# Kernel tuning notes

Measured on AMD Instinct MI355X. Metric: run time of the kernel, lower is better.

Reference implementation:

```python
import jax, jax.numpy as jnp
import numpy as np

N = 8192        # nodes
D_IN = 256      # in_dims
D_OUT = 32      # out_dims (assignment clusters)


def setup_inputs() -> dict:
    key = jax.random.key(0)
    k1, k2, k3 = jax.random.split(key, 3)
    main_feat = jax.random.normal(k1, (N, D_IN), dtype=jnp.float32)
    main_adj = jax.random.uniform(k2, (N, N), dtype=jnp.float32)
    W = jax.random.normal(k3, (D_IN, D_OUT), dtype=jnp.float32) * (1.0 / np.sqrt(D_IN))
    b = jnp.zeros((D_OUT,), dtype=jnp.float32)
    return {"main_feat": main_feat, "main_adj": main_adj, "W": W, "b": b}


def reference(main_feat, main_adj, W, b):
    # GraphConvolution: support = X @ W ; out = A @ support + b   -> [N, D_OUT]
    support = main_feat @ W
    assign = main_adj @ support + b
    # softmax over the NODE axis (dim 0), matching F.softmax(main_assign, 0)
    assign = jax.nn.softmax(assign, axis=0)
    # pooling: raw_emb = assign^T @ X  -> [D_OUT, D_IN]
    raw_emb = assign.T @ main_feat
    return raw_emb
```

## Files before the change

kernel.cpp:

```cpp
#include <hip/hip_runtime.h>
#include <stdint.h>

#define NN   8192
#define DIN  256
#define DOUT 32

typedef short bf16x8 __attribute__((ext_vector_type(8)));
typedef float f32x16 __attribute__((ext_vector_type(16)));

union BF8 { uint32_t u[4]; bf16x8 v; };

__device__ __forceinline__ void split_pair(float a, float b, uint32_t& hp, uint32_t& lp) {
    uint32_t ua = __float_as_uint(a), ub = __float_as_uint(b);
    hp = (ua >> 16) | (ub & 0xffff0000u);
    float la = a - __uint_as_float(ua & 0xffff0000u);
    float lb = b - __uint_as_float(ub & 0xffff0000u);
    lp = (__float_as_uint(la) >> 16) | (__float_as_uint(lb) & 0xffff0000u);
}

__global__ __launch_bounds__(256) void k1_support(
    const float* __restrict__ X, const float* __restrict__ W,
    unsigned short* __restrict__ hi_frag, unsigned short* __restrict__ lo_frag)
{
    __shared__ float Xs[32 * 256];
    int t = threadIdx.x;
    int kbase = blockIdx.x * 32;

    const float4* Xg = (const float4*)(X + (size_t)kbase * DIN);
    float4* Xs4 = (float4*)Xs;
#pragma unroll
    for (int p = 0; p < 8; ++p) Xs4[p * 256 + t] = Xg[p * 256 + t];
    __syncthreads();

    int c = t & 31;
    int q = t >> 5;
    int kb2  = q >> 2;
    int half = (q >> 1) & 1;
    int j4   = q & 1;
    int krow0 = kb2 * 16 + half * 8 + j4 * 4;

    float acc[4] = {0.f, 0.f, 0.f, 0.f};
    for (int d = 0; d < 256; ++d) {
        float w = W[d * 32 + c];
#pragma unroll
        for (int jj = 0; jj < 4; ++jj)
            acc[jj] += Xs[(krow0 + jj) * 256 + d] * w;
    }

    uint32_t h01, l01, h23, l23;
    split_pair(acc[0], acc[1], h01, l01);
    split_pair(acc[2], acc[3], h23, l23);

    int ks = (kbase >> 4) + kb2;
    size_t elembase = (size_t)ks * 512 + (size_t)(half * 32 + c) * 8 + j4 * 4;
    *(uint2*)(hi_frag + elembase) = make_uint2(h01, h23);
    *(uint2*)(lo_frag + elembase) = make_uint2(l01, l23);
}

__global__ __launch_bounds__(256) void k2_logits(
    const float* __restrict__ adj,
    const unsigned short* __restrict__ hi_frag,
    const unsigned short* __restrict__ lo_frag,
    float* __restrict__ part)
{
    int t = threadIdx.x;
    int lane = t & 63, wv = t >> 6;
    int row_tile = blockIdx.x * 128 + wv * 32;
    int r  = lane & 31;
    int hs = lane >> 5;

    const float* arow = adj + (size_t)(row_tile + r) * NN + blockIdx.y * 512 + hs * 8;
    const unsigned short* hp = hi_frag + (size_t)blockIdx.y * 32 * 512 + lane * 8;
    const unsigned short* lp = lo_frag + (size_t)blockIdx.y * 32 * 512 + lane * 8;

    f32x16 acc;
#pragma unroll
    for (int i = 0; i < 16; ++i) acc[i] = 0.f;

#pragma unroll 4
    for (int s = 0; s < 32; ++s) {
        float4 a0 = *(const float4*)arow;
        float4 a1 = *(const float4*)(arow + 4);
        BF8 bh, bl, ah, al;
        bh.v = *(const bf16x8*)hp;
        bl.v = *(const bf16x8*)lp;
        split_pair(a0.x, a0.y, ah.u[0], al.u[0]);
        split_pair(a0.z, a0.w, ah.u[1], al.u[1]);
        split_pair(a1.x, a1.y, ah.u[2], al.u[2]);
        split_pair(a1.z, a1.w, ah.u[3], al.u[3]);
        acc = __builtin_amdgcn_mfma_f32_32x32x16_bf16(ah.v, bh.v, acc, 0, 0, 0);
        acc = __builtin_amdgcn_mfma_f32_32x32x16_bf16(ah.v, bl.v, acc, 0, 0, 0);
        acc = __builtin_amdgcn_mfma_f32_32x32x16_bf16(al.v, bh.v, acc, 0, 0, 0);
        arow += 16; hp += 512; lp += 512;
    }

    float* pdst = part + (size_t)blockIdx.y * (NN * DOUT);
#pragma unroll
    for (int reg = 0; reg < 16; ++reg) {
        int rt = (reg & 3) + 8 * (reg >> 2) + 4 * hs;
        pdst[(size_t)(row_tile + rt) * 32 + r] = acc[reg];
    }
}

__global__ __launch_bounds__(256) void k3a_sum_max(
    const float* __restrict__ part, float* __restrict__ logits_sum,
    float* __restrict__ Mpart)
{
    __shared__ float red[256 * 4];
    int t = threadIdx.x;
    size_t base4 = (size_t)blockIdx.x * 1024;

    float mx[4] = {-3.4e38f, -3.4e38f, -3.4e38f, -3.4e38f};
#pragma unroll
    for (int k = 0; k < 4; ++k) {
        size_t f = base4 + k * 256 + t;
        float4 v = ((const float4*)part)[f];
#pragma unroll
        for (int p = 1; p < 16; ++p) {
            float4 u = ((const float4*)(part + (size_t)p * NN * DOUT))[f];
            v.x += u.x; v.y += u.y; v.z += u.z; v.w += u.w;
        }
        ((float4*)logits_sum)[f] = v;
        mx[0] = fmaxf(mx[0], v.x); mx[1] = fmaxf(mx[1], v.y);
        mx[2] = fmaxf(mx[2], v.z); mx[3] = fmaxf(mx[3], v.w);
    }
#pragma unroll
    for (int j = 0; j < 4; ++j) red[t * 4 + j] = mx[j];
    __syncthreads();
    for (int s = 128; s >= 8; s >>= 1) {
        if (t < s)
#pragma unroll
            for (int j = 0; j < 4; ++j)
                red[t * 4 + j] = fmaxf(red[t * 4 + j], red[(t + s) * 4 + j]);
        __syncthreads();
    }
    if (t < 8)
#pragma unroll
        for (int j = 0; j < 4; ++j)
            Mpart[blockIdx.x * 32 + t * 4 + j] = red[t * 4 + j];
}

__global__ __launch_bounds__(256) void k3b_exp_sum(
    const float* __restrict__ logits_sum, const float* __restrict__ Mpart,
    float* __restrict__ e_buf, float* __restrict__ Spart)
{
    __shared__ float Ms[32];
    __shared__ float red[256 * 4];
    int t = threadIdx.x;

    if (t < 32) {
        float m = -3.4e38f;
        for (int g = 0; g < 64; ++g) m = fmaxf(m, Mpart[g * 32 + t]);
        Ms[t] = m;
    }
    __syncthreads();

    int g = t & 7;
    float m0 = Ms[4 * g], m1 = Ms[4 * g + 1], m2 = Ms[4 * g + 2], m3 = Ms[4 * g + 3];
    size_t base4 = (size_t)blockIdx.x * 1024;
    float sm[4] = {0.f, 0.f, 0.f, 0.f};
#pragma unroll
    for (int k = 0; k < 4; ++k) {
        size_t f = base4 + k * 256 + t;
        float4 v = ((const float4*)logits_sum)[f];
        v.x = __expf(v.x - m0); v.y = __expf(v.y - m1);
        v.z = __expf(v.z - m2); v.w = __expf(v.w - m3);
        ((float4*)e_buf)[f] = v;
        sm[0] += v.x; sm[1] += v.y; sm[2] += v.z; sm[3] += v.w;
    }
#pragma unroll
    for (int j = 0; j < 4; ++j) red[t * 4 + j] = sm[j];
    __syncthreads();
    for (int s = 128; s >= 8; s >>= 1) {
        if (t < s)
#pragma unroll
            for (int j = 0; j < 4; ++j)
                red[t * 4 + j] += red[(t + s) * 4 + j];
        __syncthreads();
    }
    if (t < 8)
#pragma unroll
        for (int j = 0; j < 4; ++j)
            Spart[blockIdx.x * 32 + t * 4 + j] = red[t * 4 + j];
}

__global__ __launch_bounds__(256) void k4_pool(
    const float* __restrict__ X, const float* __restrict__ e_buf,
    const float* __restrict__ Spart, float* __restrict__ p4)
{
    __shared__ float Xs[8 * 256];
    __shared__ float As[8 * 32];
    __shared__ float invS[32];
    int t = threadIdx.x;
    int c = t & 31, dg = t >> 5;
    int ibase = blockIdx.x * 64;

    if (t < 32) {
        float s = 0.f;
        for (int g = 0; g < 64; ++g) s += Spart[g * 32 + t];
        invS[t] = 1.0f / s;
    }

    float acc[32];
#pragma unroll
    for (int i = 0; i < 32; ++i) acc[i] = 0.f;

    for (int rnd = 0; rnd < 8; ++rnd) {
        __syncthreads();
        const float4* Xg = (const float4*)(X + (size_t)(ibase + rnd * 8) * DIN);
        float4* Xs4 = (float4*)Xs;
        Xs4[t]       = Xg[t];
        Xs4[256 + t] = Xg[256 + t];
        As[t] = e_buf[(size_t)(ibase + rnd * 8 + (t >> 5)) * 32 + (t & 31)] * invS[t & 31];
        __syncthreads();
#pragma unroll
        for (int i2 = 0; i2 < 8; ++i2) {
            float a = As[i2 * 32 + c];
#pragma unroll
            for (int dd = 0; dd < 32; ++dd)
                acc[dd] += a * Xs[i2 * 256 + dg * 32 + dd];
        }
    }
    float* dst = p4 + (size_t)blockIdx.x * (DOUT * DIN) + (size_t)c * 256 + dg * 32;
#pragma unroll
    for (int v = 0; v < 8; ++v)
        ((float4*)dst)[v] = make_float4(acc[v * 4], acc[v * 4 + 1], acc[v * 4 + 2], acc[v * 4 + 3]);
}

__global__ __launch_bounds__(256) void k5_reduce(
    const float* __restrict__ p4, float* __restrict__ out)
{
    int j = blockIdx.x * 256 + threadIdx.x;
    float a = 0.f;
    for (int g = 0; g < 128; ++g) a += p4[(size_t)g * (DOUT * DIN) + j];
    out[j] = a;
}

extern "C" void kernel_launch(void* const* d_in, const int* in_sizes, int n_in,
                              void* d_out, int out_size, void* d_ws, size_t ws_size,
                              hipStream_t stream) {
    const float* X   = (const float*)d_in[0];
    const float* adj = (const float*)d_in[1];
    const float* W   = (const float*)d_in[2];
    float* out = (float*)d_out;

    char* w = (char*)d_ws;
    unsigned short* hi_frag = (unsigned short*)w;
    unsigned short* lo_frag = (unsigned short*)(w + 512 * 1024);
    float* part       = (float*)(w + 1 * 1024 * 1024);
    float* logits_sum = (float*)(w + 17 * 1024 * 1024);
    float* e_buf      = (float*)(w + 18 * 1024 * 1024);
    float* Mpart      = (float*)(w + 19 * 1024 * 1024);
    float* Spart      = (float*)(w + 19 * 1024 * 1024 + 8192);
    float* p4         = (float*)(w + 19 * 1024 * 1024 + 16384);

    k1_support<<<NN / 32, 256, 0, stream>>>(X, W, hi_frag, lo_frag);
    k2_logits<<<dim3(NN / 128, 16), 256, 0, stream>>>(adj, hi_frag, lo_frag, part);
    k3a_sum_max<<<64, 256, 0, stream>>>(part, logits_sum, Mpart);
    k3b_exp_sum<<<64, 256, 0, stream>>>(logits_sum, Mpart, e_buf, Spart);
    k4_pool<<<128, 256, 0, stream>>>(X, e_buf, Spart, p4);
    k5_reduce<<<DOUT * DIN / 256, 256, 0, stream>>>(p4, out);
}
```

Before: 439.3 us.

## Halve split-K chunks, widen softmax grids, defer normalization to final reduce

The adjacency GEMM now splits K into 8 chunks of 1024 instead of 16 of 512. This halves the partial-logit buffer written by k2 and read by k3a, at the cost of fewer blocks (512 instead of 1024) in the dominant kernel. The softmax max and exp kernels now run 256 blocks with one float4 per thread, and k3b reduces the 256 partial maxima with a tree. Division by the softmax sum moves from k4_pool into k5_reduce, which reduces Spart per output column and scales the result once.

Result: no change. 443.3 us (+0.9%).

```diff
diff --git a/kernel.cpp b/kernel.cpp
--- a/kernel.cpp
+++ b/kernel.cpp
@@ -4,6 +4,8 @@
 #define NN   8192
 #define DIN  256
 #define DOUT 32
+#define NCHUNK 8
+#define NP4   128
 
 typedef short bf16x8 __attribute__((ext_vector_type(8)));
 typedef float f32x16 __attribute__((ext_vector_type(16)));
@@ -69,16 +71,16 @@
     int r  = lane & 31;
     int hs = lane >> 5;
 
-    const float* arow = adj + (size_t)(row_tile + r) * NN + blockIdx.y * 512 + hs * 8;
-    const unsigned short* hp = hi_frag + (size_t)blockIdx.y * 32 * 512 + lane * 8;
-    const unsigned short* lp = lo_frag + (size_t)blockIdx.y * 32 * 512 + lane * 8;
+    const float* arow = adj + (size_t)(row_tile + r) * NN + blockIdx.y * 1024 + hs * 8;
+    const unsigned short* hp = hi_frag + (size_t)blockIdx.y * 64 * 512 + lane * 8;
+    const unsigned short* lp = lo_frag + (size_t)blockIdx.y * 64 * 512 + lane * 8;
 
     f32x16 acc;
 #pragma unroll
     for (int i = 0; i < 16; ++i) acc[i] = 0.f;
 
 #pragma unroll 4
-    for (int s = 0; s < 32; ++s) {
+    for (int s = 0; s < 64; ++s) {
         float4 a0 = *(const float4*)arow;
         float4 a1 = *(const float4*)(arow + 4);
         BF8 bh, bl, ah, al;
@@ -108,24 +110,18 @@
 {
     __shared__ float red[256 * 4];
     int t = threadIdx.x;
-    size_t base4 = (size_t)blockIdx.x * 1024;
-
-    float mx[4] = {-3.4e38f, -3.4e38f, -3.4e38f, -3.4e38f};
-#pragma unroll
-    for (int k = 0; k < 4; ++k) {
-        size_t f = base4 + k * 256 + t;
-        float4 v = ((const float4*)part)[f];
-#pragma unroll
-        for (int p = 1; p < 16; ++p) {
-            float4 u = ((const float4*)(part + (size_t)p * NN * DOUT))[f];
-            v.x += u.x; v.y += u.y; v.z += u.z; v.w += u.w;
-        }
-        ((float4*)logits_sum)[f] = v;
-        mx[0] = fmaxf(mx[0], v.x); mx[1] = fmaxf(mx[1], v.y);
-        mx[2] = fmaxf(mx[2], v.z); mx[3] = fmaxf(mx[3], v.w);
-    }
-#pragma unroll
-    for (int j = 0; j < 4; ++j) red[t * 4 + j] = mx[j];
+    size_t f = (size_t)blockIdx.x * 256 + t;
+
+    float4 v = ((const float4*)part)[f];
+#pragma unroll
+    for (int p = 1; p < NCHUNK; ++p) {
+        float4 u = ((const float4*)(part + (size_t)p * NN * DOUT))[f];
+        v.x += u.x; v.y += u.y; v.z += u.z; v.w += u.w;
+    }
+    ((float4*)logits_sum)[f] = v;
+
+    red[t * 4 + 0] = v.x; red[t * 4 + 1] = v.y;
+    red[t * 4 + 2] = v.z; red[t * 4 + 3] = v.w;
     __syncthreads();
     for (int s = 128; s >= 8; s >>= 1) {
         if (t < s)
@@ -144,32 +140,35 @@
     const float* __restrict__ logits_sum, const float* __restrict__ Mpart,
     float* __restrict__ e_buf, float* __restrict__ Spart)
 {
+    __shared__ float redm[8 * 32];
     __shared__ float Ms[32];
     __shared__ float red[256 * 4];
     int t = threadIdx.x;
-
-    if (t < 32) {
-        float m = -3.4e38f;
-        for (int g = 0; g < 64; ++g) m = fmaxf(m, Mpart[g * 32 + t]);
-        Ms[t] = m;
-    }
-    __syncthreads();
-
-    int g = t & 7;
-    float m0 = Ms[4 * g], m1 = Ms[4 * g + 1], m2 = Ms[4 * g + 2], m3 = Ms[4 * g + 3];
-    size_t base4 = (size_t)blockIdx.x * 1024;
-    float sm[4] = {0.f, 0.f, 0.f, 0.f};
-#pragma unroll
-    for (int k = 0; k < 4; ++k) {
-        size_t f = base4 + k * 256 + t;
-        float4 v = ((const float4*)logits_sum)[f];
-        v.x = __expf(v.x - m0); v.y = __expf(v.y - m1);
-        v.z = __expf(v.z - m2); v.w = __expf(v.w - m3);
-        ((float4*)e_buf)[f] = v;
-        sm[0] += v.x; sm[1] += v.y; sm[2] += v.z; sm[3] += v.w;
-    }
-#pragma unroll
-    for (int j = 0; j < 4; ++j) red[t * 4 + j] = sm[j];
+    int c = t & 31, g = t >> 5;
+
+    float m = -3.4e38f;
+#pragma unroll
+    for (int i = 0; i < 32; ++i)
+        m = fmaxf(m, Mpart[(g + 8 * i) * 32 + c]);
+    redm[g * 32 + c] = m;
+    __syncthreads();
+    for (int s = 4; s >= 1; s >>= 1) {
+        if (g < s) redm[g * 32 + c] = fmaxf(redm[g * 32 + c], redm[(g + s) * 32 + c]);
+        __syncthreads();
+    }
+    if (t < 32) Ms[t] = redm[t];
+    __syncthreads();
+
+    int cg = t & 7;
+    float m0 = Ms[4 * cg], m1 = Ms[4 * cg + 1], m2 = Ms[4 * cg + 2], m3 = Ms[4 * cg + 3];
+    size_t f = (size_t)blockIdx.x * 256 + t;
+    float4 v = ((const float4*)logits_sum)[f];
+    v.x = __expf(v.x - m0); v.y = __expf(v.y - m1);
+    v.z = __expf(v.z - m2); v.w = __expf(v.w - m3);
+    ((float4*)e_buf)[f] = v;
+
+    red[t * 4 + 0] = v.x; red[t * 4 + 1] = v.y;
+    red[t * 4 + 2] = v.z; red[t * 4 + 3] = v.w;
     __syncthreads();
     for (int s = 128; s >= 8; s >>= 1) {
         if (t < s)
@@ -186,20 +185,13 @@
 
 __global__ __launch_bounds__(256) void k4_pool(
     const float* __restrict__ X, const float* __restrict__ e_buf,
-    const float* __restrict__ Spart, float* __restrict__ p4)
+    float* __restrict__ p4)
 {
     __shared__ float Xs[8 * 256];
     __shared__ float As[8 * 32];
-    __shared__ float invS[32];
     int t = threadIdx.x;
     int c = t & 31, dg = t >> 5;
     int ibase = blockIdx.x * 64;
-
-    if (t < 32) {
-        float s = 0.f;
-        for (int g = 0; g < 64; ++g) s += Spart[g * 32 + t];
-        invS[t] = 1.0f / s;
-    }
 
     float acc[32];
 #pragma unroll
@@ -211,7 +203,7 @@
         float4* Xs4 = (float4*)Xs;
         Xs4[t]       = Xg[t];
         Xs4[256 + t] = Xg[256 + t];
-        As[t] = e_buf[(size_t)(ibase + rnd * 8 + (t >> 5)) * 32 + (t & 31)] * invS[t & 31];
+        As[t] = e_buf[(size_t)(ibase + rnd * 8 + (t >> 5)) * 32 + (t & 31)];
         __syncthreads();
 #pragma unroll
         for (int i2 = 0; i2 < 8; ++i2) {
@@ -228,12 +220,24 @@
 }
 
 __global__ __launch_bounds__(256) void k5_reduce(
-    const float* __restrict__ p4, float* __restrict__ out)
-{
-    int j = blockIdx.x * 256 + threadIdx.x;
+    const float* __restrict__ p4, const float* __restrict__ Spart,
+    float* __restrict__ out)
+{
+    __shared__ float red[256];
+    int t = threadIdx.x, b = blockIdx.x;
+
+    red[t] = Spart[t * 32 + b];
+    __syncthreads();
+    for (int s = 128; s >= 1; s >>= 1) {
+        if (t < s) red[t] += red[t + s];
+        __syncthreads();
+    }
+    float invS = 1.0f / red[0];
+
+    int j = b * 256 + t;
     float a = 0.f;
-    for (int g = 0; g < 128; ++g) a += p4[(size_t)g * (DOUT * DIN) + j];
-    out[j] = a;
+    for (int g = 0; g < NP4; ++g) a += p4[(size_t)g * (DOUT * DIN) + j];
+    out[j] = a * invS;
 }
 
 extern "C" void kernel_launch(void* const* d_in, const int* in_sizes, int n_in,
@@ -248,16 +252,16 @@
     unsigned short* hi_frag = (unsigned short*)w;
     unsigned short* lo_frag = (unsigned short*)(w + 512 * 1024);
     float* part       = (float*)(w + 1 * 1024 * 1024);
-    float* logits_sum = (float*)(w + 17 * 1024 * 1024);
-    float* e_buf      = (float*)(w + 18 * 1024 * 1024);
-    float* Mpart      = (float*)(w + 19 * 1024 * 1024);
-    float* Spart      = (float*)(w + 19 * 1024 * 1024 + 8192);
-    float* p4         = (float*)(w + 19 * 1024 * 1024 + 16384);
+    float* logits_sum = (float*)(w + 9 * 1024 * 1024);
+    float* e_buf      = (float*)(w + 10 * 1024 * 1024);
+    float* Mpart      = (float*)(w + 11 * 1024 * 1024);
+    float* Spart      = (float*)(w + 11 * 1024 * 1024 + 32768);
+    float* p4         = (float*)(w + 11 * 1024 * 1024 + 65536);
 
     k1_support<<<NN / 32, 256, 0, stream>>>(X, W, hi_frag, lo_frag);
-    k2_logits<<<dim3(NN / 128, 16), 256, 0, stream>>>(adj, hi_frag, lo_frag, part);
-    k3a_sum_max<<<64, 256, 0, stream>>>(part, logits_sum, Mpart);
-    k3b_exp_sum<<<64, 256, 0, stream>>>(logits_sum, Mpart, e_buf, Spart);
-    k4_pool<<<128, 256, 0, stream>>>(X, e_buf, Spart, p4);
-    k5_reduce<<<DOUT * DIN / 256, 256, 0, stream>>>(p4, out);
-}
+    k2_logits<<<dim3(NN / 128, NCHUNK), 256, 0, stream>>>(adj, hi_frag, lo_frag, part);
+    k3a_sum_max<<<256, 256, 0, stream>>>(part, logits_sum, Mpart);
+    k3b_exp_sum<<<256, 256, 0, stream>>>(logits_sum, Mpart, e_buf, Spart);
+    k4_pool<<<NP4, 256, 0, stream>>>(X, e_buf, p4);
+    k5_reduce<<<DOUT, 256, 0, stream>>>(p4, Spart, out);
+}
```
